# Kernel tuning notes

Measured on AMD Instinct MI355X. Metric: run time of the kernel, lower is better.

Reference implementation:

```python
import jax, jax.numpy as jnp
import numpy as np

E = 8          # num_experts
H = 2048       # hidden_size
I = 1408       # moe_intermediate_size
T = 4096       # tokens (batch*seq)
K = 2          # top_k


def setup_inputs() -> dict:
    key = jax.random.key(0)
    ks = jax.random.split(key, 6)
    hidden_states = jax.random.normal(ks[0], (T, H), dtype=jnp.float32)
    top_k_index = jax.random.randint(ks[1], (T, K), 0, E, dtype=jnp.int64)
    top_k_weights = jax.random.uniform(ks[2], (T, K), dtype=jnp.float32)
    scale = 0.02
    Wg = jax.random.normal(ks[3], (E, H, I), dtype=jnp.float32) * scale  # gate_proj per expert
    Wu = jax.random.normal(ks[4], (E, H, I), dtype=jnp.float32) * scale  # up_proj per expert
    Wd = jax.random.normal(ks[5], (E, I, H), dtype=jnp.float32) * scale  # down_proj per expert
    return {"hidden_states": hidden_states, "top_k_index": top_k_index,
            "top_k_weights": top_k_weights, "Wg": Wg, "Wu": Wu, "Wd": Wd}


def reference(hidden_states, top_k_index, top_k_weights, Wg, Wu, Wd):
    # Combine weights per (expert, token): w[e,t] = sum_k weights[t,k] * [idx[t,k]==e]
    one_hot = jax.nn.one_hot(top_k_index, E, dtype=hidden_states.dtype)  # [T,K,E]
    w = jnp.einsum('tke,tk->et', one_hot, top_k_weights)                 # [E,T]
    # SwiGLU MLP for every expert (dense masked-compute formulation of the
    # original gather->MLP->weighted scatter-add loop; identical math)
    g = jnp.einsum('th,ehi->eti', hidden_states, Wg)                     # [E,T,I]
    u = jnp.einsum('th,ehi->eti', hidden_states, Wu)                     # [E,T,I]
    y = jnp.einsum('eti,eih->eth', jax.nn.silu(g) * u, Wd)               # [E,T,H]
    # Weighted combine (scatter-add over experts)
    return jnp.einsum('et,eth->th', w, y)                                # [T,H]
```

## Files before the change

kernel.cpp:

```cpp
#include <hip/hip_runtime.h>

#define T_TOK 4096
#define H_DIM 2048
#define I_DIM 1408
#define E_NUM 8
#define NPAIR 8192
#define BM 128
#define BK 64
#define NT1 32
#define NT2 22
#define G1_BLOCKS 1584
#define G2_BLOCKS 1152
#define PREP_BLOCKS 10497

typedef float f32x4 __attribute__((ext_vector_type(4)));
typedef short s16x8 __attribute__((ext_vector_type(8)));

static __device__ __forceinline__ short f2bf(float f) {
  union { float f; unsigned u; } c; c.f = f;
  unsigned r = c.u + 0x7FFFu + ((c.u >> 16) & 1u);
  return (short)(r >> 16);
}

#define GLD16(g, l) __builtin_amdgcn_global_load_lds( \
    (const __attribute__((address_space(1))) void*)(g), \
    (__attribute__((address_space(3))) void*)(l), 16, 0, 0)

__global__ __launch_bounds__(256) void moe_prep(
    const float* __restrict__ hidden, const float* __restrict__ Wg,
    const float* __restrict__ Wu, const float* __restrict__ Wd,
    const int* __restrict__ idx, const float* __restrict__ wts,
    short* __restrict__ hb, short* __restrict__ wgt,
    short* __restrict__ wut, short* __restrict__ wdt,
    int* __restrict__ tok_s, float* __restrict__ wt_s, int* __restrict__ inv,
    int* __restrict__ tile_e, int* __restrict__ tile_r0,
    int* __restrict__ tile_r1, int* __restrict__ ntiles) {
  __shared__ float tf[64 * 128];
  __shared__ int cnt[E_NUM], cur[E_NUM];
  int b = blockIdx.x, tid = threadIdx.x;

  if (b < 2048) {
    size_t i = ((size_t)b * 256 + tid) * 16;
    const f32x4* s = (const f32x4*)(hidden + i);
    f32x4 a = s[0], bb = s[1], c = s[2], d = s[3];
    s16x8 v0, v1;
    v0[0]=f2bf(a[0]); v0[1]=f2bf(a[1]); v0[2]=f2bf(a[2]); v0[3]=f2bf(a[3]);
    v0[4]=f2bf(bb[0]); v0[5]=f2bf(bb[1]); v0[6]=f2bf(bb[2]); v0[7]=f2bf(bb[3]);
    v1[0]=f2bf(c[0]); v1[1]=f2bf(c[1]); v1[2]=f2bf(c[2]); v1[3]=f2bf(c[3]);
    v1[4]=f2bf(d[0]); v1[5]=f2bf(d[1]); v1[6]=f2bf(d[2]); v1[7]=f2bf(d[3]);
    *(s16x8*)(hb + i) = v0;
    *(s16x8*)(hb + i + 8) = v1;
    return;
  }
  if (b == PREP_BLOCKS - 1) {
    if (tid < E_NUM) cnt[tid] = 0;
    __syncthreads();
    for (int p = tid; p < NPAIR; p += 256) atomicAdd(&cnt[idx[p] & 7], 1);
    __syncthreads();
    if (tid == 0) {
      int o = 0, nt = 0;
      for (int e = 0; e < E_NUM; e++) {
        cur[e] = o;
        int c = cnt[e];
        for (int m0 = 0; m0 < c; m0 += BM) {
          tile_e[nt] = e;
          tile_r0[nt] = o + m0;
          tile_r1[nt] = o + ((m0 + BM < c) ? (m0 + BM) : c);
          nt++;
        }
        o += c;
      }
      *ntiles = nt;
    }
    __syncthreads();
    for (int p = tid; p < NPAIR; p += 256) {
      int e = idx[p] & 7;
      int pos = atomicAdd(&cur[e], 1);
      tok_s[pos] = p >> 1;
      wt_s[pos]  = wts[p];
      inv[p]     = pos;
    }
    return;
  }
  int lb = b - 2048;
  int sec = lb / 2816, s = lb % 2816;
  const float* src; short* dst; int K, N, ntn;
  if (sec == 0)      { src = Wg; dst = wgt; K = H_DIM; N = I_DIM; ntn = 11; }
  else if (sec == 1) { src = Wu; dst = wut; K = H_DIM; N = I_DIM; ntn = 11; }
  else               { src = Wd; dst = wdt; K = I_DIM; N = H_DIM; ntn = 16; }
  int e = s / 352, tile = s % 352;
  int nt = tile % ntn, kb = tile / ntn;
  src += (size_t)e * ((size_t)K * N);
  dst += (size_t)e * ((size_t)K * N);
  int lane = tid & 63, wv = tid >> 6;
  #pragma unroll
  for (int j = 0; j < 8; j++) {
    int row = wv * 16 + 2 * j + (lane >> 5);
    const float* g = src + (size_t)(kb * 64 + row) * N + nt * 128 + (lane & 31) * 4;
    GLD16(g, tf + (wv * 8 + j) * 256);
  }
  __syncthreads();
  int n = tid >> 1, h = tid & 1;
  float v[32];
  #pragma unroll
  for (int i = 0; i < 32; i++) v[i] = tf[(h * 32 + i) * 128 + n];
  s16x8 o0, o1, o2, o3;
  #pragma unroll
  for (int j = 0; j < 8; j++) {
    o0[j] = f2bf(v[j]);      o1[j] = f2bf(v[8 + j]);
    o2[j] = f2bf(v[16 + j]); o3[j] = f2bf(v[24 + j]);
  }
  short* op = dst + ((size_t)kb * N + nt * 128) * 64 + tid * 32;
  *(s16x8*)(op)      = o0;
  *(s16x8*)(op + 8)  = o1;
  *(s16x8*)(op + 16) = o2;
  *(s16x8*)(op + 24) = o3;
}

__global__ __launch_bounds__(256, 2) void moe_gemm1(
    const short* __restrict__ hb, const short* __restrict__ Wgt,
    const short* __restrict__ Wut, const int* __restrict__ tok_s,
    const int* __restrict__ tile_e, const int* __restrict__ tile_r0,
    const int* __restrict__ tile_r1, const int* __restrict__ ntiles,
    short* __restrict__ act) {
  __shared__ short As[BM * BK];
  __shared__ short Bg[64 * BK];
  __shared__ short Bu[64 * BK];
  int L = (blockIdx.x & 7) * (G1_BLOCKS / 8) + (blockIdx.x >> 3);
  int bt = L / 22;
  if (bt >= *ntiles) return;
  int e = tile_e[bt], r0 = tile_r0[bt], r1 = tile_r1[bt];
  int n0 = (L % 22) * 64;
  const short* wg = Wgt + (size_t)e * ((size_t)H_DIM * I_DIM);
  const short* wu = Wut + (size_t)e * ((size_t)H_DIM * I_DIM);

  int tid = threadIdx.x, lane = tid & 63, wv = tid >> 6;
  int l3 = lane >> 3;
  int k8 = (((lane & 7) ^ l3) << 3);

  const short *a_src[4], *g_src[2], *u_src[2];
  short *a_dst[4], *g_dst[2], *u_dst[2];
  #pragma unroll
  for (int s = 0; s < 4; s++) {
    int row = wv * 32 + s * 8 + l3;
    int p = r0 + row; if (p > NPAIR - 1) p = NPAIR - 1;
    a_src[s] = hb + (size_t)tok_s[p] * H_DIM + k8;
    a_dst[s] = As + (wv * 32 + s * 8) * BK;
  }
  #pragma unroll
  for (int s = 0; s < 2; s++) {
    int row = wv * 16 + s * 8 + l3;
    g_src[s] = wg + (size_t)(n0 + row) * 64 + k8;
    u_src[s] = wu + (size_t)(n0 + row) * 64 + k8;
    g_dst[s] = Bg + (wv * 16 + s * 8) * BK;
    u_dst[s] = Bu + (wv * 16 + s * 8) * BK;
  }

  int wm = wv >> 1, wn = wv & 1;
  int lrow = lane & 15, lk = lane >> 4;
  int ch0 = ((lk ^ (lrow & 7)) << 3);
  int ch1 = (((4 + lk) ^ (lrow & 7)) << 3);

  f32x4 accg[4][2], accu[4][2];
  #pragma unroll
  for (int i = 0; i < 4; i++)
    #pragma unroll
    for (int j = 0; j < 2; j++) { accg[i][j] = 0; accu[i][j] = 0; }

  #define G1_STAGE(t) do { int ka = (t) << 6; int kbb = (t) * (I_DIM << 6); \
    GLD16(a_src[0]+ka, a_dst[0]); GLD16(a_src[1]+ka, a_dst[1]); \
    GLD16(a_src[2]+ka, a_dst[2]); GLD16(a_src[3]+ka, a_dst[3]); \
    GLD16(g_src[0]+kbb, g_dst[0]); GLD16(g_src[1]+kbb, g_dst[1]); \
    GLD16(u_src[0]+kbb, u_dst[0]); GLD16(u_src[1]+kbb, u_dst[1]); } while (0)

  #define G1_RD(ch, af, bgf, buf_) do { \
    _Pragma("unroll") \
    for (int mf = 0; mf < 4; mf++) \
      af[mf] = *(const s16x8*)&As[(wm * 64 + mf * 16 + lrow) * BK + (ch)]; \
    _Pragma("unroll") \
    for (int nf = 0; nf < 2; nf++) { \
      int oo = (wn * 32 + nf * 16 + lrow) * BK + (ch); \
      bgf[nf] = *(const s16x8*)&Bg[oo]; \
      buf_[nf] = *(const s16x8*)&Bu[oo]; } } while (0)

  #define G1_MFMA(af, bgf, buf_) do { \
    _Pragma("unroll") \
    for (int mf = 0; mf < 4; mf++) \
      _Pragma("unroll") \
      for (int nf = 0; nf < 2; nf++) { \
        accg[mf][nf] = __builtin_amdgcn_mfma_f32_16x16x32_bf16(af[mf], bgf[nf], accg[mf][nf], 0, 0, 0); \
        accu[mf][nf] = __builtin_amdgcn_mfma_f32_16x16x32_bf16(af[mf], buf_[nf], accu[mf][nf], 0, 0, 0); } } while (0)

  G1_STAGE(0);
  __syncthreads();
  for (int t = 0; t < NT1 - 1; ++t) {
    s16x8 a0[4], bg0[2], bu0[2];
    G1_RD(ch0, a0, bg0, bu0);
    G1_MFMA(a0, bg0, bu0);
    s16x8 a1[4], bg1[2], bu1[2];
    G1_RD(ch1, a1, bg1, bu1);
    __syncthreads();
    G1_STAGE(t + 1);
    __builtin_amdgcn_sched_barrier(0);
    G1_MFMA(a1, bg1, bu1);
    __syncthreads();
  }
  {
    s16x8 a0[4], bg0[2], bu0[2];
    G1_RD(ch0, a0, bg0, bu0);
    G1_MFMA(a0, bg0, bu0);
    s16x8 a1[4], bg1[2], bu1[2];
    G1_RD(ch1, a1, bg1, bu1);
    G1_MFMA(a1, bg1, bu1);
  }

  #pragma unroll
  for (int mf = 0; mf < 4; mf++) {
    int rb = r0 + wm * 64 + mf * 16 + (lk << 2);
    #pragma unroll
    for (int nf = 0; nf < 2; nf++) {
      int col = n0 + wn * 32 + nf * 16 + lrow;
      #pragma unroll
      for (int j = 0; j < 4; j++) {
        int p = rb + j;
        if (p < r1) {
          float g = accg[mf][nf][j], u = accu[mf][nf][j];
          float s = g / (1.f + __expf(-g)) * u;
          act[p * I_DIM + col] = f2bf(s);
        }
      }
    }
  }
}

__global__ __launch_bounds__(256, 2) void moe_gemm2(
    const short* __restrict__ act, const short* __restrict__ Wdt,
    const int* __restrict__ tile_e, const int* __restrict__ tile_r0,
    const int* __restrict__ tile_r1, const int* __restrict__ ntiles,
    float* __restrict__ y) {
  __shared__ short As[BM * BK];
  __shared__ short Bd[BM * BK];
  int L = (blockIdx.x & 7) * (G2_BLOCKS / 8) + (blockIdx.x >> 3);
  int bt = L >> 4;
  if (bt >= *ntiles) return;
  int e = tile_e[bt], r0 = tile_r0[bt], r1 = tile_r1[bt];
  int n0 = (L & 15) * 128;
  const short* wd = Wdt + (size_t)e * ((size_t)H_DIM * I_DIM);

  int tid = threadIdx.x, lane = tid & 63, wv = tid >> 6;
  int l3 = lane >> 3;
  int k8 = (((lane & 7) ^ l3) << 3);

  const short *a_src[4], *b_src[4];
  short *a_dst[4], *b_dst[4];
  #pragma unroll
  for (int s = 0; s < 4; s++) {
    int row = wv * 32 + s * 8 + l3;
    int p = r0 + row; if (p > NPAIR - 1) p = NPAIR - 1;
    a_src[s] = act + (size_t)p * I_DIM + k8;
    b_src[s] = wd + (size_t)(n0 + row) * 64 + k8;
    a_dst[s] = As + (wv * 32 + s * 8) * BK;
    b_dst[s] = Bd + (wv * 32 + s * 8) * BK;
  }

  int wm = wv >> 1, wn = wv & 1;
  int lrow = lane & 15, lk = lane >> 4;
  int ch0 = ((lk ^ (lrow & 7)) << 3);
  int ch1 = (((4 + lk) ^ (lrow & 7)) << 3);

  f32x4 acc[4][4];
  #pragma unroll
  for (int i = 0; i < 4; i++)
    #pragma unroll
    for (int j = 0; j < 4; j++) acc[i][j] = 0;

  #define G2_STAGE(t) do { int ka = (t) << 6; int kbb = (t) * (H_DIM << 6); \
    GLD16(a_src[0]+ka, a_dst[0]); GLD16(a_src[1]+ka, a_dst[1]); \
    GLD16(a_src[2]+ka, a_dst[2]); GLD16(a_src[3]+ka, a_dst[3]); \
    GLD16(b_src[0]+kbb, b_dst[0]); GLD16(b_src[1]+kbb, b_dst[1]); \
    GLD16(b_src[2]+kbb, b_dst[2]); GLD16(b_src[3]+kbb, b_dst[3]); } while (0)

  #define G2_RD(ch, af, bf) do { \
    _Pragma("unroll") \
    for (int mf = 0; mf < 4; mf++) \
      af[mf] = *(const s16x8*)&As[(wm * 64 + mf * 16 + lrow) * BK + (ch)]; \
    _Pragma("unroll") \
    for (int nf = 0; nf < 4; nf++) \
      bf[nf] = *(const s16x8*)&Bd[(wn * 64 + nf * 16 + lrow) * BK + (ch)]; } while (0)

  #define G2_MFMA(af, bf) do { \
    _Pragma("unroll") \
    for (int mf = 0; mf < 4; mf++) \
      _Pragma("unroll") \
      for (int nf = 0; nf < 4; nf++) \
        acc[mf][nf] = __builtin_amdgcn_mfma_f32_16x16x32_bf16(af[mf], bf[nf], acc[mf][nf], 0, 0, 0); } while (0)

  G2_STAGE(0);
  __syncthreads();
  for (int t = 0; t < NT2 - 1; ++t) {
    s16x8 a0[4], b0[4];
    G2_RD(ch0, a0, b0);
    G2_MFMA(a0, b0);
    s16x8 a1[4], b1[4];
    G2_RD(ch1, a1, b1);
    __syncthreads();
    G2_STAGE(t + 1);
    __builtin_amdgcn_sched_barrier(0);
    G2_MFMA(a1, b1);
    __syncthreads();
  }
  {
    s16x8 a0[4], b0[4];
    G2_RD(ch0, a0, b0);
    G2_MFMA(a0, b0);
    s16x8 a1[4], b1[4];
    G2_RD(ch1, a1, b1);
    G2_MFMA(a1, b1);
  }

  #pragma unroll
  for (int mf = 0; mf < 4; mf++) {
    int rb = r0 + wm * 64 + mf * 16 + (lk << 2);
    #pragma unroll
    for (int nf = 0; nf < 4; nf++) {
      int col = n0 + wn * 64 + nf * 16 + lrow;
      #pragma unroll
      for (int j = 0; j < 4; j++) {
        int p = rb + j;
        if (p < r1) {
          y[(size_t)p * H_DIM + col] = acc[mf][nf][j];
        }
      }
    }
  }
}

__global__ __launch_bounds__(256) void moe_combine(
    const float* __restrict__ y, const int* __restrict__ inv,
    const float* __restrict__ wt_s, float* __restrict__ out) {
  int t = blockIdx.x;
  int p0 = inv[2 * t], p1 = inv[2 * t + 1];
  float w0 = wt_s[p0], w1 = wt_s[p1];
  const f32x4* y0 = (const f32x4*)(y + (size_t)p0 * H_DIM);
  const f32x4* y1 = (const f32x4*)(y + (size_t)p1 * H_DIM);
  f32x4* o = (f32x4*)(out + (size_t)t * H_DIM);
  int i = threadIdx.x;
  f32x4 a0 = y0[i], b0 = y1[i];
  f32x4 a1 = y0[i + 256], b1 = y1[i + 256];
  o[i] = w0 * a0 + w1 * b0;
  o[i + 256] = w0 * a1 + w1 * b1;
}

extern "C" void kernel_launch(void* const* d_in, const int* in_sizes, int n_in,
                              void* d_out, int out_size, void* d_ws, size_t ws_size,
                              hipStream_t stream) {
  const float* hidden = (const float*)d_in[0];
  const int*   idx    = (const int*)d_in[1];
  const float* wts    = (const float*)d_in[2];
  const float* Wg     = (const float*)d_in[3];
  const float* Wu     = (const float*)d_in[4];
  const float* Wd     = (const float*)d_in[5];
  float* out = (float*)d_out;

  char* ws = (char*)d_ws;
  int*   tok_s   = (int*)(ws);
  float* wt_s    = (float*)(ws + 32768);
  int*   tile_e  = (int*)(ws + 65536);
  int*   tile_r0 = (int*)(ws + 66048);
  int*   tile_r1 = (int*)(ws + 66560);
  int*   ntiles  = (int*)(ws + 67072);
  int*   inv     = (int*)(ws + 131072);

  const size_t OFF_HB  = 1ull << 20;
  const size_t OFF_WGT = OFF_HB  + 16777216ull;
  const size_t OFF_WUT = OFF_WGT + 46137344ull;
  const size_t OFF_WDT = OFF_WUT + 46137344ull;
  const size_t OFF_ACT = OFF_WDT + 46137344ull;

  short* hb  = (short*)(ws + OFF_HB);
  short* wgt = (short*)(ws + OFF_WGT);
  short* wut = (short*)(ws + OFF_WUT);
  short* wdt = (short*)(ws + OFF_WDT);
  short* act = (short*)(ws + OFF_ACT);
  float* y   = (float*)(ws + OFF_WGT);

  moe_prep<<<PREP_BLOCKS, 256, 0, stream>>>(hidden, Wg, Wu, Wd, idx, wts,
      hb, wgt, wut, wdt, tok_s, wt_s, inv, tile_e, tile_r0, tile_r1, ntiles);
  moe_gemm1<<<G1_BLOCKS, 256, 0, stream>>>(hb, wgt, wut, tok_s,
      tile_e, tile_r0, tile_r1, ntiles, act);
  moe_gemm2<<<G2_BLOCKS, 256, 0, stream>>>(act, wdt,
      tile_e, tile_r0, tile_r1, ntiles, y);
  moe_combine<<<T_TOK, 256, 0, stream>>>(y, inv, wt_s, out);
}
```

Baseline: 312.6 us.

## Double-buffer weight transpose strips per k-block in prep kernel

Each weight-transpose block in the prep kernel now handles a whole 64-row k-block and loops over all column strips, instead of launching one block per 64x128 tile. Two LDS buffers let the async global-to-LDS load of the next strip overlap the bf16 conversion and store of the current strip. This cuts the prep grid from about 10.5k blocks to about 2.7k and saves per-block launch and sync overhead. The cost is double the LDS per block, which lowers occupancy, and a coarser work split that can leave a load-imbalanced tail across CUs.

New measurement: 305.2 us. 2.4% less time.

```diff
diff --git a/kernel.cpp b/kernel.cpp
--- a/kernel.cpp
+++ b/kernel.cpp
@@ -11,7 +11,7 @@
 #define NT2 22
 #define G1_BLOCKS 1584
 #define G2_BLOCKS 1152
-#define PREP_BLOCKS 10497
+#define PREP_BLOCKS 2737
 
 typedef float f32x4 __attribute__((ext_vector_type(4)));
 typedef short s16x8 __attribute__((ext_vector_type(8)));
@@ -35,7 +35,7 @@
     int* __restrict__ tok_s, float* __restrict__ wt_s, int* __restrict__ inv,
     int* __restrict__ tile_e, int* __restrict__ tile_r0,
     int* __restrict__ tile_r1, int* __restrict__ ntiles) {
-  __shared__ float tf[64 * 128];
+  __shared__ float tf[2][8192];
   __shared__ int cnt[E_NUM], cur[E_NUM];
   int b = blockIdx.x, tid = threadIdx.x;
 
@@ -83,38 +83,55 @@
     return;
   }
   int lb = b - 2048;
-  int sec = lb / 2816, s = lb % 2816;
-  const float* src; short* dst; int K, N, ntn;
-  if (sec == 0)      { src = Wg; dst = wgt; K = H_DIM; N = I_DIM; ntn = 11; }
-  else if (sec == 1) { src = Wu; dst = wut; K = H_DIM; N = I_DIM; ntn = 11; }
-  else               { src = Wd; dst = wdt; K = I_DIM; N = H_DIM; ntn = 16; }
-  int e = s / 352, tile = s % 352;
-  int nt = tile % ntn, kb = tile / ntn;
-  src += (size_t)e * ((size_t)K * N);
-  dst += (size_t)e * ((size_t)K * N);
+  const float* src; short* dst; int N, kb, nstrips;
+  if (lb < 512) {
+    src = (lb < 256) ? Wg : Wu;
+    dst = (lb < 256) ? wgt : wut;
+    int l = lb & 255;
+    int e = l >> 5; kb = l & 31;
+    N = I_DIM; nstrips = 11;
+    src += (size_t)e * ((size_t)H_DIM * I_DIM);
+    dst += (size_t)e * ((size_t)H_DIM * I_DIM);
+  } else {
+    int l = lb - 512;
+    int e = l / 22; kb = l % 22;
+    src = Wd; dst = wdt; N = H_DIM; nstrips = 16;
+    src += (size_t)e * ((size_t)I_DIM * H_DIM);
+    dst += (size_t)e * ((size_t)I_DIM * H_DIM);
+  }
   int lane = tid & 63, wv = tid >> 6;
-  #pragma unroll
-  for (int j = 0; j < 8; j++) {
-    int row = wv * 16 + 2 * j + (lane >> 5);
-    const float* g = src + (size_t)(kb * 64 + row) * N + nt * 128 + (lane & 31) * 4;
-    GLD16(g, tf + (wv * 8 + j) * 256);
-  }
+  int srow = wv * 16 + (lane >> 5);
+  const float* g0 = src + (size_t)(kb * 64 + srow) * N + (lane & 31) * 4;
+
+  #define TSTAGE(buf, strip) do { \
+    const float* gs = g0 + (strip) * 128; \
+    float* ld = (buf) + (wv * 8) * 256; \
+    _Pragma("unroll") \
+    for (int j = 0; j < 8; j++) \
+      GLD16(gs + (size_t)(2 * j) * N, ld + j * 256); } while (0)
+
+  int n = tid >> 1, h = tid & 1;
+  TSTAGE(tf[0], 0);
   __syncthreads();
-  int n = tid >> 1, h = tid & 1;
-  float v[32];
-  #pragma unroll
-  for (int i = 0; i < 32; i++) v[i] = tf[(h * 32 + i) * 128 + n];
-  s16x8 o0, o1, o2, o3;
-  #pragma unroll
-  for (int j = 0; j < 8; j++) {
-    o0[j] = f2bf(v[j]);      o1[j] = f2bf(v[8 + j]);
-    o2[j] = f2bf(v[16 + j]); o3[j] = f2bf(v[24 + j]);
-  }
-  short* op = dst + ((size_t)kb * N + nt * 128) * 64 + tid * 32;
-  *(s16x8*)(op)      = o0;
-  *(s16x8*)(op + 8)  = o1;
-  *(s16x8*)(op + 16) = o2;
-  *(s16x8*)(op + 24) = o3;
+  for (int sj = 0; sj < nstrips; sj++) {
+    if (sj + 1 < nstrips) TSTAGE(tf[(sj + 1) & 1], sj + 1);
+    const float* tb = tf[sj & 1];
+    float v[32];
+    #pragma unroll
+    for (int i = 0; i < 32; i++) v[i] = tb[(h * 32 + i) * 128 + n];
+    s16x8 o0, o1, o2, o3;
+    #pragma unroll
+    for (int j = 0; j < 8; j++) {
+      o0[j] = f2bf(v[j]);      o1[j] = f2bf(v[8 + j]);
+      o2[j] = f2bf(v[16 + j]); o3[j] = f2bf(v[24 + j]);
+    }
+    short* op = dst + ((size_t)kb * N + sj * 128) * 64 + tid * 32;
+    *(s16x8*)(op)      = o0;
+    *(s16x8*)(op + 8)  = o1;
+    *(s16x8*)(op + 16) = o2;
+    *(s16x8*)(op + 24) = o3;
+    __syncthreads();
+  }
 }
 
 __global__ __launch_bounds__(256, 2) void moe_gemm1(
```
